# Kernel optimization log

Hardware: AMD Instinct MI355X
Metric: run time of the kernel (lower is better)

Reference implementation:

```python
import jax, jax.numpy as jnp
import numpy as np

N = 100000          # nodes
E = 1600000         # edges
F_IN = 128          # in_channels
C = 32              # hidden_channels (per head)
H = 4               # heads
NEG_SLOPE = 0.2     # PyG GATConv default leaky_relu slope


def setup_inputs() -> dict:
    key = jax.random.key(0)
    ks = jax.random.split(key, 6)
    x = jax.random.normal(ks[0], (N, F_IN), dtype=jnp.float32)
    edge_index = jax.random.randint(ks[1], (2, E), 0, N, dtype=jnp.int32)
    # learned params (PyG GATConv: lin weight, att_src, att_dst, bias)
    W = jax.random.normal(ks[2], (F_IN, H * C), dtype=jnp.float32) * (1.0 / np.sqrt(F_IN))
    att_src = jax.random.normal(ks[3], (H, C), dtype=jnp.float32) * 0.1
    att_dst = jax.random.normal(ks[4], (H, C), dtype=jnp.float32) * 0.1
    bias = jnp.zeros((H * C,), dtype=jnp.float32)
    return {"x": x, "edge_index": edge_index, "W": W,
            "att_src": att_src, "att_dst": att_dst, "bias": bias}


def reference(x, edge_index, W, att_src, att_dst, bias):
    # linear projection, split into heads: [N, H, C]
    h = (x @ W).reshape(N, H, C)
    # per-node attention terms: [N, H]
    a_src = jnp.einsum('nhc,hc->nh', h, att_src)
    a_dst = jnp.einsum('nhc,hc->nh', h, att_dst)
    src, dst = edge_index[0], edge_index[1]
    # edge-wise logits: [E, H]
    alpha = jax.nn.leaky_relu(a_src[src] + a_dst[dst], NEG_SLOPE)
    # segment softmax over incoming edges of each dst node
    amax = jax.ops.segment_max(alpha, dst, num_segments=N)       # [N, H]
    amax = jnp.where(jnp.isfinite(amax), amax, 0.0)
    ex = jnp.exp(alpha - amax[dst])                              # [E, H]
    denom = jax.ops.segment_sum(ex, dst, num_segments=N)         # [N, H]
    alpha = ex / (denom[dst] + 1e-16)                            # [E, H]
    # weighted messages, scatter-add to dst: [N, H, C]
    msg = h[src] * alpha[:, :, None]
    out = jax.ops.segment_sum(msg, dst, num_segments=N)
    out = out.reshape(N, H * C) + bias
    return jax.nn.elu(out)
```

## Files before the change

### kernel.cpp

```cpp
#include <hip/hip_runtime.h>
#include <hip/hip_bf16.h>
#include <math.h>

#define N_NODES 100000
#define N_EDGES 1600000
#define NEG_SLOPE 0.2f

#define NB_BUCKET 782
#define ST_CAP 2560

#define OFF_H     0
#define OFF_ASRC  25600000
#define OFF_ADST  27200000
#define OFF_NODE  28800000
#define OFF_BCUR  29600000
#define OFF_TMP   29604096
#define OFF_WHT   37611776
#define OFF_WLT   37644544

typedef __attribute__((ext_vector_type(8))) __bf16 bf16x8;
typedef __attribute__((ext_vector_type(4))) float  f32x4;
union BF8 { unsigned u32[4]; bf16x8 v; };

__device__ __forceinline__ float leaky(float x) {
    return fmaxf(x, NEG_SLOPE * x);
}
__device__ __forceinline__ float sel4(int h, float a, float b, float c, float d) {
    return h == 0 ? a : (h == 1 ? b : (h == 2 ? c : d));
}
__device__ __forceinline__ float2 bf2_to_f2(unsigned int u) {
    float2 r;
    r.x = __uint_as_float(u << 16);
    r.y = __uint_as_float(u & 0xffff0000u);
    return r;
}
__device__ __forceinline__ unsigned bf16_rne(float f) {
    const unsigned b = __float_as_uint(f);
    return ((b + 0x7FFFu + ((b >> 16) & 1u)) >> 16) & 0xFFFFu;
}
__device__ __forceinline__ float bf16_tof(unsigned hb) {
    return __uint_as_float(hb << 16);
}
__device__ __forceinline__ void wave_lds_fence() {
    asm volatile("s_waitcnt lgkmcnt(0)" ::: "memory");
    __builtin_amdgcn_sched_barrier(0);
}

__global__ __launch_bounds__(256) void wprep_kernel(
    const float* __restrict__ W, ushort* __restrict__ WhT, ushort* __restrict__ WlT)
{
    const int idx = blockIdx.x * 256 + threadIdx.x;
    const int n = idx >> 7, k = idx & 127;
    const float w  = W[k * 128 + n];
    const unsigned hb = bf16_rne(w);
    const float rs = w - bf16_tof(hb);
    const unsigned lb = bf16_rne(rs);
    WhT[n * 128 + k] = (ushort)hb;
    WlT[n * 128 + k] = (ushort)lb;
}

__global__ __launch_bounds__(256, 2) void gemm_mfma_kernel(
    const float* __restrict__ x, const ushort* __restrict__ WhT,
    const ushort* __restrict__ WlT,
    const float* __restrict__ att_src, const float* __restrict__ att_dst,
    ushort* __restrict__ h_u16, float* __restrict__ a_src, float* __restrict__ a_dst)
{
    const int wv   = threadIdx.x >> 6;
    const int lane = threadIdx.x & 63;
    const int c15  = lane & 15;
    const int kg   = lane >> 4;
    const int r0g  = blockIdx.x * 128 + wv * 32;

    bf16x8 ah[2][4], al[2][4];
#pragma unroll
    for (int mt = 0; mt < 2; ++mt) {
        int row = r0g + mt * 16 + c15;
        row = row < N_NODES ? row : N_NODES - 1;
        const float4* xp = (const float4*)&x[(size_t)row * 128];
#pragma unroll
        for (int ks = 0; ks < 4; ++ks) {
            const int kb = ks * 32 + kg * 8;
            const float4 fa = xp[kb >> 2];
            const float4 fb = xp[(kb >> 2) + 1];
            const float f[8] = {fa.x, fa.y, fa.z, fa.w, fb.x, fb.y, fb.z, fb.w};
            BF8 H, L;
#pragma unroll
            for (int j = 0; j < 4; ++j) {
                const unsigned h0 = bf16_rne(f[2 * j + 0]);
                const unsigned h1 = bf16_rne(f[2 * j + 1]);
                const unsigned l0 = bf16_rne(f[2 * j + 0] - bf16_tof(h0));
                const unsigned l1 = bf16_rne(f[2 * j + 1] - bf16_tof(h1));
                H.u32[j] = h0 | (h1 << 16);
                L.u32[j] = l0 | (l1 << 16);
            }
            ah[mt][ks] = H.v;
            al[mt][ks] = L.v;
        }
    }

    f32x4 acc[2][8];
#pragma unroll
    for (int mt = 0; mt < 2; ++mt)
#pragma unroll
        for (int nt = 0; nt < 8; ++nt)
            acc[mt][nt] = (f32x4){0.f, 0.f, 0.f, 0.f};

#pragma unroll
    for (int ks = 0; ks < 4; ++ks) {
        const int kb = ks * 32 + kg * 8;
#pragma unroll
        for (int nt = 0; nt < 8; ++nt) {
            const int col = nt * 16 + c15;
            const bf16x8 bh = *(const bf16x8*)&WhT[col * 128 + kb];
            const bf16x8 bl = *(const bf16x8*)&WlT[col * 128 + kb];
            acc[0][nt] = __builtin_amdgcn_mfma_f32_16x16x32_bf16(ah[0][ks], bh, acc[0][nt], 0, 0, 0);
            acc[1][nt] = __builtin_amdgcn_mfma_f32_16x16x32_bf16(ah[1][ks], bh, acc[1][nt], 0, 0, 0);
            acc[0][nt] = __builtin_amdgcn_mfma_f32_16x16x32_bf16(al[0][ks], bh, acc[0][nt], 0, 0, 0);
            acc[1][nt] = __builtin_amdgcn_mfma_f32_16x16x32_bf16(al[1][ks], bh, acc[1][nt], 0, 0, 0);
            acc[0][nt] = __builtin_amdgcn_mfma_f32_16x16x32_bf16(ah[0][ks], bl, acc[0][nt], 0, 0, 0);
            acc[1][nt] = __builtin_amdgcn_mfma_f32_16x16x32_bf16(ah[1][ks], bl, acc[1][nt], 0, 0, 0);
        }
    }

    float asv[8], adv[8];
#pragma unroll
    for (int nt = 0; nt < 8; ++nt) {
        asv[nt] = att_src[nt * 16 + c15];
        adv[nt] = att_dst[nt * 16 + c15];
    }
#pragma unroll
    for (int mt = 0; mt < 2; ++mt) {
#pragma unroll
        for (int reg = 0; reg < 4; ++reg) {
            const int row = r0g + mt * 16 + kg * 4 + reg;
            const bool ok = row < N_NODES;
            if (ok) {
#pragma unroll
                for (int nt = 0; nt < 8; ++nt)
                    h_u16[(size_t)row * 128 + nt * 16 + c15] =
                        (ushort)bf16_rne(acc[mt][nt][reg]);
            }
            float ps[4], pd[4];
#pragma unroll
            for (int hh = 0; hh < 4; ++hh) {
                ps[hh] = acc[mt][2 * hh][reg] * asv[2 * hh] +
                         acc[mt][2 * hh + 1][reg] * asv[2 * hh + 1];
                pd[hh] = acc[mt][2 * hh][reg] * adv[2 * hh] +
                         acc[mt][2 * hh + 1][reg] * adv[2 * hh + 1];
            }
#pragma unroll
            for (int off = 1; off < 16; off <<= 1) {
#pragma unroll
                for (int hh = 0; hh < 4; ++hh) {
                    ps[hh] += __shfl_xor(ps[hh], off);
                    pd[hh] += __shfl_xor(pd[hh], off);
                }
            }
            if (ok && c15 == 0) {
#pragma unroll
                for (int hh = 0; hh < 4; ++hh) {
                    a_src[row * 4 + hh] = ps[hh];
                    a_dst[row * 4 + hh] = pd[hh];
                }
            }
        }
    }
}

#define S1_EPB 6250
__global__ __launch_bounds__(256) void scat_kernel(
    const int* __restrict__ src, const int* __restrict__ dst,
    int* __restrict__ bcur, unsigned int* __restrict__ tmp)
{
    __shared__ int cnt[NB_BUCKET];
    const int tid = threadIdx.x;
    for (int i = tid; i < NB_BUCKET; i += 256) cnt[i] = 0;
    __syncthreads();
    const int e0 = blockIdx.x * S1_EPB;
    for (int i = tid; i < S1_EPB; i += 256)
        atomicAdd(&cnt[dst[e0 + i] >> 7], 1);
    __syncthreads();
    for (int b = tid; b < NB_BUCKET; b += 256) {
        const int c = cnt[b];
        cnt[b] = c ? (b * ST_CAP + atomicAdd(&bcur[b], c)) : 0;
    }
    __syncthreads();
    for (int i = tid; i < S1_EPB; i += 256) {
        const int d = dst[e0 + i];
        const int s = src[e0 + i];
        const int p = atomicAdd(&cnt[d >> 7], 1);
        tmp[p] = ((unsigned int)s << 7) | (unsigned int)(d & 127);
    }
}

__global__ __launch_bounds__(256) void phaseB_kernel(
    const unsigned int* __restrict__ tmp, const int* __restrict__ bcur,
    int2* __restrict__ node_info, int* __restrict__ csr)
{
    __shared__ unsigned int st[ST_CAP];
    __shared__ int hist[128];
    __shared__ int cur[128];
    __shared__ int wtot[4];

    const int b    = blockIdx.x;
    const int tid  = threadIdx.x;
    const int lane = tid & 63;
    const int wv   = tid >> 6;
    const int base = b * ST_CAP;
    int cnt = bcur[b];
    cnt = cnt < ST_CAP ? cnt : ST_CAP;

    if (tid < 128) hist[tid] = 0;
    __syncthreads();

    for (int i = tid; i < cnt; i += 256) {
        const unsigned int v = tmp[base + i];
        st[i] = v;
        atomicAdd(&hist[v & 127], 1);
    }
    __syncthreads();

    const int hv = (tid < 128) ? hist[tid] : 0;
    int sv = hv;
#pragma unroll
    for (int off = 1; off < 64; off <<= 1) {
        int u = __shfl_up(sv, off);
        if (lane >= off) sv += u;
    }
    if (lane == 63) wtot[wv] = sv;
    __syncthreads();
    const int wpre = (wv > 0 ? wtot[0] : 0) + (wv > 1 ? wtot[1] : 0) + (wv > 2 ? wtot[2] : 0);
    if (tid < 128) {
        const int excl = wpre + sv - hv;
        cur[tid] = excl;
        const int node = (b << 7) + tid;
        if (node < N_NODES) node_info[node] = make_int2(base + excl, hv);
    }
    __syncthreads();

    for (int i = tid; i < cnt; i += 256) {
        const unsigned int v = st[i];
        const int p = atomicAdd(&cur[v & 127], 1);
        csr[base + p] = (int)(v >> 7);
    }
}

__global__ __launch_bounds__(256, 4) void gat_agg_kernel(
    const int* __restrict__ csr_src, const int2* __restrict__ node_info,
    const __hip_bfloat162* __restrict__ h_bf,
    const float* __restrict__ a_src, const float* __restrict__ a_dst,
    const float* __restrict__ bias, float* __restrict__ out)
{
    __shared__ float4 stage[4][128];

    const int wv   = threadIdx.x >> 6;
    const int lane = threadIdx.x & 63;
    const int node = blockIdx.x * 4 + wv;

    const int2 nf  = node_info[node];
    const int start = nf.x;
    const int deg   = nf.y;

    const float4 ad4 = ((const float4*)a_dst)[node];

    float sf = __int_as_float(0);
    float e0 = 0.f, e1 = 0.f, e2 = 0.f, e3 = 0.f;
    if (lane < deg) {
        const int s = csr_src[start + lane];
        sf = __int_as_float(s);
        const float4 as4 = ((const float4*)a_src)[s];
        e0 = __expf(leaky(as4.x + ad4.x));
        e1 = __expf(leaky(as4.y + ad4.y));
        e2 = __expf(leaky(as4.z + ad4.z));
        e3 = __expf(leaky(as4.w + ad4.w));
    }
    stage[wv][lane * 2 + 0] = make_float4(sf, e0, sf, e1);
    stage[wv][lane * 2 + 1] = make_float4(sf, e2, sf, e3);
    wave_lds_fence();

    if (deg <= 64) {
        const int qw   = lane >> 4;
        const int cpos = lane & 15;
        const int hsub = cpos >> 2;
        const float2* sp = (const float2*)&stage[wv][0];
        const uint4*  hp = (const uint4*)h_bf;

        float acc[8];
#pragma unroll
        for (int i = 0; i < 8; ++i) acc[i] = 0.f;
        float den = 0.f;

        for (int j = 0; j < deg; j += 16) {
#pragma unroll
            for (int u = 0; u < 4; ++u) {
                const float2 se = sp[(j + u * 4 + qw) * 4 + hsub];
                const float ev = se.y;
                const unsigned s = (unsigned)__float_as_int(se.x);
                const uint4 hv = hp[(size_t)(s * 16u + (unsigned)cpos)];
                float2 f;
                f = bf2_to_f2(hv.x);
                acc[0] = fmaf(ev, f.x, acc[0]);
                acc[1] = fmaf(ev, f.y, acc[1]);
                f = bf2_to_f2(hv.y);
                acc[2] = fmaf(ev, f.x, acc[2]);
                acc[3] = fmaf(ev, f.y, acc[3]);
                f = bf2_to_f2(hv.z);
                acc[4] = fmaf(ev, f.x, acc[4]);
                acc[5] = fmaf(ev, f.y, acc[5]);
                f = bf2_to_f2(hv.w);
                acc[6] = fmaf(ev, f.x, acc[6]);
                acc[7] = fmaf(ev, f.y, acc[7]);
                den += ev;
            }
        }

#pragma unroll
        for (int i = 0; i < 8; ++i) acc[i] += __shfl_xor(acc[i], 16);
#pragma unroll
        for (int i = 0; i < 8; ++i) acc[i] += __shfl_xor(acc[i], 32);
        den += __shfl_xor(den, 16);
        den += __shfl_xor(den, 32);

        const float inv = 1.0f / (den + 1e-16f);
#pragma unroll
        for (int i = 0; i < 8; ++i) acc[i] *= inv;

        if (qw == 0) {
            float4* sf4 = (float4*)&stage[wv][0];
            sf4[cpos * 2 + 0] = make_float4(acc[0], acc[1], acc[2], acc[3]);
            sf4[cpos * 2 + 1] = make_float4(acc[4], acc[5], acc[6], acc[7]);
        }
        wave_lds_fence();
        const float2 v  = ((const float2*)&stage[wv][0])[lane];
        const float2 b2 = ((const float2*)bias)[lane];
        float ox = v.x + b2.x;
        float oy = v.y + b2.y;
        ox = ox > 0.f ? ox : __expf(ox) - 1.f;
        oy = oy > 0.f ? oy : __expf(oy) - 1.f;
        ((float2*)out)[(size_t)node * 64 + lane] = make_float2(ox, oy);
    } else {
        const int hidx = lane >> 4;
        const float adh = sel4(hidx, ad4.x, ad4.y, ad4.z, ad4.w);
        float2 acc = {0.f, 0.f};
        float  den = 0.f;
        for (int j = 0; j < deg; ++j) {
            const int s = csr_src[start + j];
            const float ash = a_src[s * 4 + hidx];
            const float ex = __expf(leaky(ash + adh));
            const float2 f = __bfloat1622float2(h_bf[(size_t)s * 64 + lane]);
            acc.x += ex * f.x;
            acc.y += ex * f.y;
            den   += ex;
        }
        const float inv = 1.0f / (den + 1e-16f);
        const float2 b2 = ((const float2*)bias)[lane];
        float ox = acc.x * inv + b2.x;
        float oy = acc.y * inv + b2.y;
        ox = ox > 0.f ? ox : expm1f(ox);
        oy = oy > 0.f ? oy : expm1f(oy);
        ((float2*)out)[(size_t)node * 64 + lane] = make_float2(ox, oy);
    }
}

extern "C" void kernel_launch(void* const* d_in, const int* in_sizes, int n_in,
                              void* d_out, int out_size, void* d_ws, size_t ws_size,
                              hipStream_t stream)
{
    const float* x       = (const float*)d_in[0];
    const int*   ei      = (const int*)  d_in[1];
    const float* W       = (const float*)d_in[2];
    const float* att_src = (const float*)d_in[3];
    const float* att_dst = (const float*)d_in[4];
    const float* bias    = (const float*)d_in[5];
    float*       out     = (float*)d_out;

    char* ws = (char*)d_ws;
    ushort* h_u16 = (ushort*)(ws + OFF_H);
    __hip_bfloat162* h_bf = (__hip_bfloat162*)(ws + OFF_H);
    float* a_src = (float*)(ws + OFF_ASRC);
    float* a_dst = (float*)(ws + OFF_ADST);
    int2*  ninfo = (int2*) (ws + OFF_NODE);
    int*   bcur  = (int*)  (ws + OFF_BCUR);
    unsigned int* tmp = (unsigned int*)(ws + OFF_TMP);
    int*   csr   = (int*)  (ws + OFF_TMP);
    ushort* WhT  = (ushort*)(ws + OFF_WHT);
    ushort* WlT  = (ushort*)(ws + OFF_WLT);

    const int* srcp = ei;
    const int* dstp = ei + N_EDGES;

    hipMemsetAsync(bcur, 0, NB_BUCKET * sizeof(int), stream);

    wprep_kernel<<<64, 256, 0, stream>>>(W, WhT, WlT);

    gemm_mfma_kernel<<<(N_NODES + 127) / 128, 256, 0, stream>>>(
        x, WhT, WlT, att_src, att_dst, h_u16, a_src, a_dst);

    scat_kernel<<<N_EDGES / S1_EPB, 256, 0, stream>>>(srcp, dstp, bcur, tmp);
    phaseB_kernel<<<NB_BUCKET, 256, 0, stream>>>(tmp, bcur, ninfo, csr);

    gat_agg_kernel<<<N_NODES / 4, 256, 0, stream>>>(
        csr, ninfo, h_bf, a_src, a_dst, bias, out);
}
```

Baseline: 272.4 us.

## Fold attention vectors into weights as extra MFMA tile, fuse memset, stash dst in LDS

Precomputes W·att_src and W·att_dst as an extra 16-column bf16 hi/lo weight tile so a_src/a_dst come out of MFMA instead of a shuffle reduction after the GEMM. It also zeroes the bucket counters inside wprep instead of issuing a separate memset. In scat_kernel the dst indices are cached in shared memory so they are not re-read from global. Risks are slightly different rounding of the attention terms and higher LDS use in scat, which may lower occupancy.

```diff
diff --git a/kernel.cpp b/kernel.cpp
--- a/kernel.cpp
+++ b/kernel.cpp
@@ -17,6 +17,8 @@
 #define OFF_TMP   29604096
 #define OFF_WHT   37611776
 #define OFF_WLT   37644544
+#define OFF_WAH   37677312
+#define OFF_WAL   37681408
 
 typedef __attribute__((ext_vector_type(8))) __bf16 bf16x8;
 typedef __attribute__((ext_vector_type(4))) float  f32x4;
@@ -47,22 +49,41 @@
 }
 
 __global__ __launch_bounds__(256) void wprep_kernel(
-    const float* __restrict__ W, ushort* __restrict__ WhT, ushort* __restrict__ WlT)
+    const float* __restrict__ W, const float* __restrict__ att_src,
+    const float* __restrict__ att_dst,
+    ushort* __restrict__ WhT, ushort* __restrict__ WlT,
+    ushort* __restrict__ WAh, ushort* __restrict__ WAl,
+    int* __restrict__ bcur)
 {
     const int idx = blockIdx.x * 256 + threadIdx.x;
     const int n = idx >> 7, k = idx & 127;
     const float w  = W[k * 128 + n];
     const unsigned hb = bf16_rne(w);
     const float rs = w - bf16_tof(hb);
-    const unsigned lb = bf16_rne(rs);
     WhT[n * 128 + k] = (ushort)hb;
-    WlT[n * 128 + k] = (ushort)lb;
+    WlT[n * 128 + k] = (ushort)bf16_rne(rs);
+
+    if (idx < 2048) {
+        const int j = idx >> 7;
+        float v = 0.f;
+        if (j < 8) {
+            const int hh = j & 3;
+            const float* att = (j < 4) ? att_src : att_dst;
+#pragma unroll
+            for (int c = 0; c < 32; ++c)
+                v = fmaf(W[k * 128 + hh * 32 + c], att[hh * 32 + c], v);
+        }
+        const unsigned ab = bf16_rne(v);
+        WAh[j * 128 + k] = (ushort)ab;
+        WAl[j * 128 + k] = (ushort)bf16_rne(v - bf16_tof(ab));
+    }
+    if (idx < NB_BUCKET) bcur[idx] = 0;
 }
 
 __global__ __launch_bounds__(256, 2) void gemm_mfma_kernel(
     const float* __restrict__ x, const ushort* __restrict__ WhT,
-    const ushort* __restrict__ WlT,
-    const float* __restrict__ att_src, const float* __restrict__ att_dst,
+    const ushort* __restrict__ WlT, const ushort* __restrict__ WAh,
+    const ushort* __restrict__ WAl,
     ushort* __restrict__ h_u16, float* __restrict__ a_src, float* __restrict__ a_dst)
 {
     const int wv   = threadIdx.x >> 6;
@@ -99,11 +120,14 @@
     }
 
     f32x4 acc[2][8];
-#pragma unroll
-    for (int mt = 0; mt < 2; ++mt)
+    f32x4 acca[2];
+#pragma unroll
+    for (int mt = 0; mt < 2; ++mt) {
+        acca[mt] = (f32x4){0.f, 0.f, 0.f, 0.f};
 #pragma unroll
         for (int nt = 0; nt < 8; ++nt)
             acc[mt][nt] = (f32x4){0.f, 0.f, 0.f, 0.f};
+    }
 
 #pragma unroll
     for (int ks = 0; ks < 4; ++ks) {
@@ -120,49 +144,30 @@
             acc[0][nt] = __builtin_amdgcn_mfma_f32_16x16x32_bf16(ah[0][ks], bl, acc[0][nt], 0, 0, 0);
             acc[1][nt] = __builtin_amdgcn_mfma_f32_16x16x32_bf16(ah[1][ks], bl, acc[1][nt], 0, 0, 0);
         }
-    }
-
-    float asv[8], adv[8];
-#pragma unroll
-    for (int nt = 0; nt < 8; ++nt) {
-        asv[nt] = att_src[nt * 16 + c15];
-        adv[nt] = att_dst[nt * 16 + c15];
-    }
+        const bf16x8 bha = *(const bf16x8*)&WAh[c15 * 128 + kb];
+        const bf16x8 bla = *(const bf16x8*)&WAl[c15 * 128 + kb];
+        acca[0] = __builtin_amdgcn_mfma_f32_16x16x32_bf16(ah[0][ks], bha, acca[0], 0, 0, 0);
+        acca[1] = __builtin_amdgcn_mfma_f32_16x16x32_bf16(ah[1][ks], bha, acca[1], 0, 0, 0);
+        acca[0] = __builtin_amdgcn_mfma_f32_16x16x32_bf16(al[0][ks], bha, acca[0], 0, 0, 0);
+        acca[1] = __builtin_amdgcn_mfma_f32_16x16x32_bf16(al[1][ks], bha, acca[1], 0, 0, 0);
+        acca[0] = __builtin_amdgcn_mfma_f32_16x16x32_bf16(ah[0][ks], bla, acca[0], 0, 0, 0);
+        acca[1] = __builtin_amdgcn_mfma_f32_16x16x32_bf16(ah[1][ks], bla, acca[1], 0, 0, 0);
+    }
+
 #pragma unroll
     for (int mt = 0; mt < 2; ++mt) {
 #pragma unroll
         for (int reg = 0; reg < 4; ++reg) {
             const int row = r0g + mt * 16 + kg * 4 + reg;
-            const bool ok = row < N_NODES;
-            if (ok) {
-#pragma unroll
-                for (int nt = 0; nt < 8; ++nt)
-                    h_u16[(size_t)row * 128 + nt * 16 + c15] =
-                        (ushort)bf16_rne(acc[mt][nt][reg]);
-            }
-            float ps[4], pd[4];
-#pragma unroll
-            for (int hh = 0; hh < 4; ++hh) {
-                ps[hh] = acc[mt][2 * hh][reg] * asv[2 * hh] +
-                         acc[mt][2 * hh + 1][reg] * asv[2 * hh + 1];
-                pd[hh] = acc[mt][2 * hh][reg] * adv[2 * hh] +
-                         acc[mt][2 * hh + 1][reg] * adv[2 * hh + 1];
-            }
-#pragma unroll
-            for (int off = 1; off < 16; off <<= 1) {
-#pragma unroll
-                for (int hh = 0; hh < 4; ++hh) {
-                    ps[hh] += __shfl_xor(ps[hh], off);
-                    pd[hh] += __shfl_xor(pd[hh], off);
-                }
-            }
-            if (ok && c15 == 0) {
-#pragma unroll
-                for (int hh = 0; hh < 4; ++hh) {
-                    a_src[row * 4 + hh] = ps[hh];
-                    a_dst[row * 4 + hh] = pd[hh];
-                }
-            }
+            if (row >= N_NODES) continue;
+#pragma unroll
+            for (int nt = 0; nt < 8; ++nt)
+                h_u16[(size_t)row * 128 + nt * 16 + c15] =
+                    (ushort)bf16_rne(acc[mt][nt][reg]);
+            if (c15 < 4)
+                a_src[row * 4 + c15] = acca[mt][reg];
+            else if (c15 < 8)
+                a_dst[row * 4 + (c15 - 4)] = acca[mt][reg];
         }
     }
 }
@@ -173,12 +178,16 @@
     int* __restrict__ bcur, unsigned int* __restrict__ tmp)
 {
     __shared__ int cnt[NB_BUCKET];
+    __shared__ int dstash[S1_EPB];
     const int tid = threadIdx.x;
     for (int i = tid; i < NB_BUCKET; i += 256) cnt[i] = 0;
     __syncthreads();
     const int e0 = blockIdx.x * S1_EPB;
-    for (int i = tid; i < S1_EPB; i += 256)
-        atomicAdd(&cnt[dst[e0 + i] >> 7], 1);
+    for (int i = tid; i < S1_EPB; i += 256) {
+        const int d = dst[e0 + i];
+        dstash[i] = d;
+        atomicAdd(&cnt[d >> 7], 1);
+    }
     __syncthreads();
     for (int b = tid; b < NB_BUCKET; b += 256) {
         const int c = cnt[b];
@@ -186,7 +195,7 @@
     }
     __syncthreads();
     for (int i = tid; i < S1_EPB; i += 256) {
-        const int d = dst[e0 + i];
+        const int d = dstash[i];
         const int s = src[e0 + i];
         const int p = atomicAdd(&cnt[d >> 7], 1);
         tmp[p] = ((unsigned int)s << 7) | (unsigned int)(d & 127);
@@ -385,16 +394,16 @@
     int*   csr   = (int*)  (ws + OFF_TMP);
     ushort* WhT  = (ushort*)(ws + OFF_WHT);
     ushort* WlT  = (ushort*)(ws + OFF_WLT);
+    ushort* WAh  = (ushort*)(ws + OFF_WAH);
+    ushort* WAl  = (ushort*)(ws + OFF_WAL);
 
     const int* srcp = ei;
     const int* dstp = ei + N_EDGES;
 
-    hipMemsetAsync(bcur, 0, NB_BUCKET * sizeof(int), stream);
-
-    wprep_kernel<<<64, 256, 0, stream>>>(W, WhT, WlT);
+    wprep_kernel<<<64, 256, 0, stream>>>(W, att_src, att_dst, WhT, WlT, WAh, WAl, bcur);
 
     gemm_mfma_kernel<<<(N_NODES + 127) / 128, 256, 0, stream>>>(
-        x, WhT, WlT, att_src, att_dst, h_u16, a_src, a_dst);
+        x, WhT, WlT, WAh, WAl, h_u16, a_src, a_dst);
 
     scat_kernel<<<N_EDGES / S1_EPB, 256, 0, stream>>>(srcp, dstp, bcur, tmp);
     phaseB_kernel<<<NB_BUCKET, 256, 0, stream>>>(tmp, bcur, ninfo, csr);
```

Measured after the change: 268.8 us. No clear change (-1.3%).
